# Kernel tuning notes

Hardware: AMD Instinct MI355X
Metric: run time of the kernel (lower is better)

Reference implementation:

```python
import jax, jax.numpy as jnp
import numpy as np

D_MODEL = 1024
N_HEADS = 16
D_HEAD = D_MODEL // N_HEADS
D_FF = 4096
EPS = 1e-5


def _layernorm(x, g, b):
    mu = jnp.mean(x, axis=-1, keepdims=True)
    var = jnp.mean(jnp.square(x - mu), axis=-1, keepdims=True)
    return (x - mu) * jax.lax.rsqrt(var + EPS) * g + b


def setup_inputs() -> dict:
    key = jax.random.key(0)
    ks = jax.random.split(key, 16)
    B, S, D = 2, 2048, D_MODEL

    def xavier(k, shape):
        fan_in, fan_out = shape[0], shape[1]
        lim = float(np.sqrt(6.0 / (fan_in + fan_out)))
        return jax.random.uniform(k, shape, jnp.float32, -lim, lim)

    return {
        "x": jax.random.normal(ks[0], (B, S, D), jnp.float32),
        "ln1_g": jnp.ones((D,), jnp.float32),
        "ln1_b": jnp.zeros((D,), jnp.float32),
        "wq": xavier(ks[1], (D, D)), "bq": jnp.zeros((D,), jnp.float32),
        "wk": xavier(ks[2], (D, D)), "bk": jnp.zeros((D,), jnp.float32),
        "wv": xavier(ks[3], (D, D)), "bv": jnp.zeros((D,), jnp.float32),
        "wo": xavier(ks[4], (D, D)), "bo": jnp.zeros((D,), jnp.float32),
        "wf": xavier(ks[5], (D, N_HEADS)), "bf": jnp.zeros((N_HEADS,), jnp.float32),
        "ln2_g": jnp.ones((D,), jnp.float32),
        "ln2_b": jnp.zeros((D,), jnp.float32),
        "w1": xavier(ks[6], (D, D_FF)), "b1": jnp.zeros((D_FF,), jnp.float32),
        "w2": xavier(ks[7], (D_FF, D)), "b2": jnp.zeros((D,), jnp.float32),
    }


def reference(x, ln1_g, ln1_b, wq, bq, wk, bk, wv, bv, wo, bo, wf, bf,
              ln2_g, ln2_b, w1, b1, w2, b2):
    B, S, D = x.shape
    H, Dh = N_HEADS, D_HEAD

    # --- pre-norm forgetting attention ---
    h = _layernorm(x, ln1_g, ln1_b)
    q = (h @ wq + bq).reshape(B, S, H, Dh)
    k = (h @ wk + bk).reshape(B, S, H, Dh)
    v = (h @ wv + bv).reshape(B, S, H, Dh)

    # per-head scalar forget gate f_t in (0,1); cumulative log-decay c_t
    logf = jax.nn.log_sigmoid(h @ wf + bf)           # (B, S, H)
    c = jnp.cumsum(logf, axis=1)                     # (B, S, H)

    scale = 1.0 / jnp.sqrt(jnp.asarray(Dh, x.dtype))
    logits = jnp.einsum("bihd,bjhd->bhij", q, k) * scale
    # decay bias D_ij = c_i - c_j (sum of log forget gates in (j, i])
    decay = c.transpose(0, 2, 1)                     # (B, H, S)
    logits = logits + decay[:, :, :, None] - decay[:, :, None, :]

    causal = jnp.tril(jnp.ones((S, S), bool))
    logits = jnp.where(causal[None, None], logits, -jnp.inf)

    attn = jax.nn.softmax(logits, axis=-1)           # (B, H, S, S)
    ctx = jnp.einsum("bhij,bjhd->bihd", attn, v).reshape(B, S, D)
    attn_out = ctx @ wo + bo

    x = x + attn_out                                 # dropout = identity (eval)

    # --- pre-norm GELU MLP ---
    h2 = _layernorm(x, ln2_g, ln2_b)
    ff = jax.nn.gelu(h2 @ w1 + b1, approximate=False) @ w2 + b2
    return x + ff
```

## Files before the change

### kernel.cpp

```cpp
#include <hip/hip_runtime.h>
#include <hip/hip_bf16.h>
#include <math.h>

typedef unsigned short u16;
typedef unsigned int u32;
typedef __bf16 bf16x8 __attribute__((ext_vector_type(8)));
typedef float f32x4 __attribute__((ext_vector_type(4)));
typedef u32 u32x4 __attribute__((ext_vector_type(4)));

__device__ __forceinline__ u16 f2bf(float f) {
  __hip_bfloat16 h = __float2bfloat16(f);
  return *reinterpret_cast<u16*>(&h);
}
__device__ __forceinline__ float bf2f(u16 u) {
  return __uint_as_float(((u32)u) << 16);
}

#define GLL(gp, lp)                                                     \
  __builtin_amdgcn_global_load_lds(                                     \
      (const __attribute__((address_space(1))) void*)(gp),              \
      (__attribute__((address_space(3))) void*)(lp), 16, 0, 0)

__global__ __launch_bounds__(256) void transpose_cast(
    const float* __restrict__ in, u16* __restrict__ out, int R, int C) {
  __shared__ float tile[32][33];
  int c0 = blockIdx.x * 32, r0 = blockIdx.y * 32;
  int tx = threadIdx.x & 31, ty = threadIdx.x >> 5;
  for (int i = ty; i < 32; i += 8) {
    int r = r0 + i, c = c0 + tx;
    if (r < R && c < C) tile[i][tx] = in[(size_t)r * C + c];
  }
  __syncthreads();
  for (int i = ty; i < 32; i += 8) {
    int c = c0 + i, r = r0 + tx;
    if (c < C && r < R) out[(size_t)c * R + r] = f2bf(tile[tx][i]);
  }
}

__global__ __launch_bounds__(256) void pack3(
    const float* __restrict__ a, const float* __restrict__ b,
    const float* __restrict__ c, float* __restrict__ o, u32* __restrict__ ctr) {
  int t = blockIdx.x * 256 + threadIdx.x;
  if (t == 0) *ctr = 0u;
  if (t < 1024) o[t] = a[t];
  else if (t < 2048) o[t] = b[t - 1024];
  else if (t < 3072) o[t] = c[t - 2048];
}

__global__ __launch_bounds__(256) void ln_kernel(
    const float* __restrict__ x, const float* __restrict__ g,
    const float* __restrict__ bb, u16* __restrict__ out) {
  __shared__ float red[8];
  const int row = blockIdx.x;
  const float* xr = x + (size_t)row * 1024;
  f32x4 v = *(const f32x4*)(xr + threadIdx.x * 4);
  float s = v[0] + v[1] + v[2] + v[3];
  #pragma unroll
  for (int off = 32; off > 0; off >>= 1) s += __shfl_xor(s, off, 64);
  if ((threadIdx.x & 63) == 0) red[threadIdx.x >> 6] = s;
  __syncthreads();
  float mu = (red[0] + red[1] + red[2] + red[3]) * (1.0f / 1024.0f);
  f32x4 d;
  d[0] = v[0] - mu; d[1] = v[1] - mu; d[2] = v[2] - mu; d[3] = v[3] - mu;
  float sq = d[0]*d[0] + d[1]*d[1] + d[2]*d[2] + d[3]*d[3];
  #pragma unroll
  for (int off = 32; off > 0; off >>= 1) sq += __shfl_xor(sq, off, 64);
  if ((threadIdx.x & 63) == 0) red[4 + (threadIdx.x >> 6)] = sq;
  __syncthreads();
  float var = (red[4] + red[5] + red[6] + red[7]) * (1.0f / 1024.0f);
  float rstd = rsqrtf(var + 1e-5f);
  int cb = threadIdx.x * 4;
  #pragma unroll
  for (int e = 0; e < 4; ++e)
    out[(size_t)row * 1024 + cb + e] = f2bf(d[e] * rstd * g[cb + e] + bb[cb + e]);
}

__global__ __launch_bounds__(256) void gemm_bt(
    const u16* __restrict__ A, const u16* __restrict__ Bt,
    const float* __restrict__ bias, const float* __restrict__ res,
    void* __restrict__ outp, int M, int N, int K, int mode) {
  __shared__ u16 As[128 * 32];
  __shared__ u16 Bs[128 * 32];
  const int tid = threadIdx.x;
  const int m0 = blockIdx.y * 128, n0 = blockIdx.x * 128;
  const int wave = tid >> 6, lane = tid & 63;
  const int wm = (wave >> 1) * 64, wn = (wave & 1) * 64;
  const int lr = lane & 15, quad = lane >> 4;
  const int g0 = wave * 2;
  const int srow0 = g0 * 16 + (lane >> 2);
  const int scol = (lane & 3) * 8;
  const u16* Ag0 = A + (size_t)(m0 + srow0) * K + scol;
  const u16* Ag1 = A + (size_t)(m0 + srow0 + 16) * K + scol;
  const u16* Bg0 = Bt + (size_t)(n0 + srow0) * K + scol;
  const u16* Bg1 = Bt + (size_t)(n0 + srow0 + 16) * K + scol;
  u16* Al0 = As + g0 * 512;
  u16* Al1 = As + (g0 + 1) * 512;
  u16* Bl0 = Bs + g0 * 512;
  u16* Bl1 = Bs + (g0 + 1) * 512;

  f32x4 acc[4][4] = {};

  for (int k0 = 0; k0 < K; k0 += 32) {
    GLL(Ag0 + k0, Al0);
    GLL(Ag1 + k0, Al1);
    GLL(Bg0 + k0, Bl0);
    GLL(Bg1 + k0, Bl1);
    __syncthreads();
    bf16x8 af[4], bfr[4];
    #pragma unroll
    for (int t = 0; t < 4; ++t) {
      af[t]  = *(const bf16x8*)&As[(wm + t * 16 + lr) * 32 + quad * 8];
      bfr[t] = *(const bf16x8*)&Bs[(wn + t * 16 + lr) * 32 + quad * 8];
    }
    #pragma unroll
    for (int mt = 0; mt < 4; ++mt)
      #pragma unroll
      for (int nt = 0; nt < 4; ++nt)
        acc[mt][nt] = __builtin_amdgcn_mfma_f32_16x16x32_bf16(
            af[mt], bfr[nt], acc[mt][nt], 0, 0, 0);
    __syncthreads();
  }

  #pragma unroll
  for (int mt = 0; mt < 4; ++mt) {
    #pragma unroll
    for (int nt = 0; nt < 4; ++nt) {
      const int col = n0 + wn + nt * 16 + lr;
      const float bvv = bias[col];
      #pragma unroll
      for (int rr = 0; rr < 4; ++rr) {
        const int row = m0 + wm + mt * 16 + quad * 4 + rr;
        const size_t idx = (size_t)row * N + col;
        float v = acc[mt][nt][rr] + bvv;
        if (mode == 0) {
          ((float*)outp)[idx] = v;
        } else if (mode == 1) {
          ((float*)outp)[idx] = v + res[idx];
        } else if (mode == 2) {
          float gl = 0.5f * v * (1.0f + erff(v * 0.70710678118654752f));
          ((u16*)outp)[idx] = f2bf(gl);
        } else {
          ((u16*)outp)[idx] = f2bf(v);
        }
      }
    }
  }
}

__global__ __launch_bounds__(256) void gemm_n64(
    const u16* __restrict__ A, const u16* __restrict__ Bt,
    const float* __restrict__ bias, const float* __restrict__ res,
    void* __restrict__ outp, int M, int N, int K, int mode) {
  __shared__ u16 As[128 * 32];
  __shared__ u16 Bs[64 * 32];
  const int tid = threadIdx.x;
  const int m0 = blockIdx.y * 128, n0 = blockIdx.x * 64;
  const int wave = tid >> 6, lane = tid & 63;
  const int wm = (wave >> 1) * 64, wn = (wave & 1) * 32;
  const int lr = lane & 15, quad = lane >> 4;
  const int g0 = wave * 2;
  const int srow = lane >> 2;
  const int scol = (lane & 3) * 8;
  const u16* Ag0 = A + (size_t)(m0 + g0 * 16 + srow) * K + scol;
  const u16* Ag1 = A + (size_t)(m0 + g0 * 16 + 16 + srow) * K + scol;
  const u16* Bg  = Bt + (size_t)(n0 + wave * 16 + srow) * K + scol;
  u16* Al0 = As + g0 * 512;
  u16* Al1 = As + (g0 + 1) * 512;
  u16* Bl  = Bs + wave * 512;

  f32x4 acc[4][2] = {};

  for (int k0 = 0; k0 < K; k0 += 32) {
    GLL(Ag0 + k0, Al0);
    GLL(Ag1 + k0, Al1);
    GLL(Bg + k0, Bl);
    __syncthreads();
    bf16x8 af[4], bfr[2];
    #pragma unroll
    for (int t = 0; t < 4; ++t)
      af[t] = *(const bf16x8*)&As[(wm + t * 16 + lr) * 32 + quad * 8];
    #pragma unroll
    for (int t = 0; t < 2; ++t)
      bfr[t] = *(const bf16x8*)&Bs[(wn + t * 16 + lr) * 32 + quad * 8];
    #pragma unroll
    for (int mt = 0; mt < 4; ++mt)
      #pragma unroll
      for (int nt = 0; nt < 2; ++nt)
        acc[mt][nt] = __builtin_amdgcn_mfma_f32_16x16x32_bf16(
            af[mt], bfr[nt], acc[mt][nt], 0, 0, 0);
    __syncthreads();
  }

  #pragma unroll
  for (int mt = 0; mt < 4; ++mt) {
    #pragma unroll
    for (int nt = 0; nt < 2; ++nt) {
      const int col = n0 + wn + nt * 16 + lr;
      const float bvv = bias[col];
      #pragma unroll
      for (int rr = 0; rr < 4; ++rr) {
        const int row = m0 + wm + mt * 16 + quad * 4 + rr;
        const size_t idx = (size_t)row * N + col;
        float v = acc[mt][nt][rr] + bvv;
        if (mode == 0) {
          ((float*)outp)[idx] = v;
        } else if (mode == 1) {
          ((float*)outp)[idx] = v + res[idx];
        } else if (mode == 2) {
          float gl = 0.5f * v * (1.0f + erff(v * 0.70710678118654752f));
          ((u16*)outp)[idx] = f2bf(gl);
        } else {
          ((u16*)outp)[idx] = f2bf(v);
        }
      }
    }
  }
}

__global__ __launch_bounds__(64) void logf_kernel(
    const u16* __restrict__ h, const u16* __restrict__ wfT,
    const float* __restrict__ bfv, float* __restrict__ c) {
  const int row = blockIdx.x;
  const int lane = threadIdx.x;
  float acc[16];
  #pragma unroll
  for (int n = 0; n < 16; ++n) acc[n] = 0.f;
  for (int t = 0; t < 16; ++t) {
    int kidx = t * 64 + lane;
    float hv = bf2f(h[(size_t)row * 1024 + kidx]);
    #pragma unroll
    for (int n = 0; n < 16; ++n)
      acc[n] += hv * bf2f(wfT[n * 1024 + kidx]);
  }
  float z = 0.f;
  #pragma unroll
  for (int n = 0; n < 16; ++n) {
    float r = acc[n];
    #pragma unroll
    for (int off = 1; off < 64; off <<= 1) r += __shfl_xor(r, off, 64);
    if (lane == n) z = r;
  }
  if (lane < 16) {
    z += bfv[lane];
    float lf = (z >= 0.f) ? -log1pf(expf(-z)) : (z - log1pf(expf(z)));
    c[(size_t)row * 16 + lane] = lf;
  }
}

__global__ __launch_bounds__(64) void cumsum_kernel(float* __restrict__ c, int S) {
  const int b = blockIdx.x >> 4, h = blockIdx.x & 15;
  const int lane = threadIdx.x;
  float carry = 0.f;
  for (int s0 = 0; s0 < S; s0 += 64) {
    float v = c[(size_t)(b * S + s0 + lane) * 16 + h];
    #pragma unroll
    for (int off = 1; off < 64; off <<= 1) {
      float t = __shfl_up(v, off, 64);
      if (lane >= off) v += t;
    }
    v += carry;
    c[(size_t)(b * S + s0 + lane) * 16 + h] = v;
    carry = __shfl(v, 63, 64);
  }
}

__global__ __launch_bounds__(256) void vtrans(
    const u16* __restrict__ qkvb, u16* __restrict__ vtg) {
  __shared__ u16 t[32][33];
  const int bh = blockIdx.z, b = bh >> 4, h = bh & 15;
  const int s0 = blockIdx.x * 32, d0 = blockIdx.y * 32;
  const int tx = threadIdx.x & 31, ty = threadIdx.x >> 5;
  for (int i = ty; i < 32; i += 8)
    t[i][tx] = qkvb[(size_t)(b * 2048 + s0 + i) * 3072 + 2048 + h * 64 + d0 + tx];
  __syncthreads();
  for (int i = ty; i < 32; i += 8)
    vtg[(size_t)(bh * 64 + d0 + i) * 2048 + s0 + tx] = t[tx][i];
}

#define FS 72
#define NITEMS 1024

__global__ __launch_bounds__(256) void fattn(
    const u16* __restrict__ qkvb, const u16* __restrict__ vtg,
    const float* __restrict__ c, u16* __restrict__ ctx, u32* __restrict__ ctr) {
  __shared__ u16 Qs[64 * FS];
  __shared__ u16 Ks[64 * FS];
  __shared__ u16 Vt[64 * FS];
  __shared__ u16 Ps[64 * FS];
  __shared__ float cjs[64];
  __shared__ u32 sh_item;
  const int S = 2048;
  const int tid = threadIdx.x, wave = tid >> 6, lane = tid & 63;
  const int lr = lane & 15, quad = lane >> 4;
  const int w16 = wave * 16;

  for (;;) {
    if (tid == 0) sh_item = atomicAdd(ctr, 1u);
    __syncthreads();
    const u32 item = sh_item;
    if (item >= NITEMS) return;
    const int qt = 31 - (int)(item >> 5);
    const int bh = (int)(item & 31), b = bh >> 4, h = bh & 15;
    const int i0 = qt * 64;

    {
      const int r = tid >> 2, cc = (tid & 3) * 16;
      const u16* src = qkvb + (size_t)(b * S + i0 + r) * 3072 + h * 64 + cc;
      *(u32x4*)&Qs[r * FS + cc] = *(const u32x4*)src;
      *(u32x4*)&Qs[r * FS + cc + 8] = *(const u32x4*)(src + 8);
    }
    float ci[4], m_[4], l_[4], alpha[4];
    f32x4 o_[4];
    #pragma unroll
    for (int r = 0; r < 4; ++r) {
      ci[r] = c[(size_t)(b * S + i0 + w16 + quad * 4 + r) * 16 + h];
      m_[r] = -INFINITY;
      l_[r] = 0.f;
    }
    #pragma unroll
    for (int dt = 0; dt < 4; ++dt) o_[dt] = (f32x4){0.f, 0.f, 0.f, 0.f};

    const int ntiles = qt + 1;
    for (int jt = 0; jt < ntiles; ++jt) {
      const int j0 = jt * 64;
      __syncthreads();
      {
        const int r = tid >> 2, cc = (tid & 3) * 16;
        const u16* ks = qkvb + (size_t)(b * S + j0 + r) * 3072 + 1024 + h * 64 + cc;
        *(u32x4*)&Ks[r * FS + cc] = *(const u32x4*)ks;
        *(u32x4*)&Ks[r * FS + cc + 8] = *(const u32x4*)(ks + 8);
        const u16* vs = vtg + (size_t)(bh * 64 + r) * 2048 + j0 + cc;
        *(u32x4*)&Vt[r * FS + cc] = *(const u32x4*)vs;
        *(u32x4*)&Vt[r * FS + cc + 8] = *(const u32x4*)(vs + 8);
        if (tid < 64) cjs[tid] = c[(size_t)(b * S + j0 + tid) * 16 + h];
      }
      __syncthreads();

      bf16x8 aq0 = *(const bf16x8*)&Qs[(w16 + lr) * FS + quad * 8];
      bf16x8 aq1 = *(const bf16x8*)&Qs[(w16 + lr) * FS + 32 + quad * 8];
      f32x4 sc[4];
      #pragma unroll
      for (int nt = 0; nt < 4; ++nt) {
        bf16x8 bk0 = *(const bf16x8*)&Ks[(nt * 16 + lr) * FS + quad * 8];
        bf16x8 bk1 = *(const bf16x8*)&Ks[(nt * 16 + lr) * FS + 32 + quad * 8];
        f32x4 z = {0.f, 0.f, 0.f, 0.f};
        z = __builtin_amdgcn_mfma_f32_16x16x32_bf16(aq0, bk0, z, 0, 0, 0);
        z = __builtin_amdgcn_mfma_f32_16x16x32_bf16(aq1, bk1, z, 0, 0, 0);
        sc[nt] = z;
      }
      const bool diag = (jt == qt);
      #pragma unroll
      for (int r = 0; r < 4; ++r) {
        const int i = i0 + w16 + quad * 4 + r;
        float lg[4], mrow = -INFINITY;
        #pragma unroll
        for (int nt = 0; nt < 4; ++nt) {
          const int j = j0 + nt * 16 + lr;
          float v = sc[nt][r] * 0.125f + ci[r] - cjs[nt * 16 + lr];
          if (diag && (j > i)) v = -INFINITY;
          lg[nt] = v;
          mrow = fmaxf(mrow, v);
        }
        #pragma unroll
        for (int off = 1; off < 16; off <<= 1)
          mrow = fmaxf(mrow, __shfl_xor(mrow, off, 64));
        const float mn = fmaxf(m_[r], mrow);
        alpha[r] = __expf(m_[r] - mn);
        m_[r] = mn;
        float rs = 0.f;
        #pragma unroll
        for (int nt = 0; nt < 4; ++nt) {
          const float p = __expf(lg[nt] - mn);
          Ps[(w16 + quad * 4 + r) * FS + nt * 16 + lr] = f2bf(p);
          rs += p;
        }
        #pragma unroll
        for (int off = 1; off < 16; off <<= 1) rs += __shfl_xor(rs, off, 64);
        l_[r] = l_[r] * alpha[r] + rs;
      }
      asm volatile("s_waitcnt lgkmcnt(0)" ::: "memory");
      #pragma unroll
      for (int dt = 0; dt < 4; ++dt)
        #pragma unroll
        for (int r = 0; r < 4; ++r) o_[dt][r] *= alpha[r];
      bf16x8 ap0 = *(const bf16x8*)&Ps[(w16 + lr) * FS + quad * 8];
      bf16x8 ap1 = *(const bf16x8*)&Ps[(w16 + lr) * FS + 32 + quad * 8];
      #pragma unroll
      for (int dt = 0; dt < 4; ++dt) {
        bf16x8 bv0 = *(const bf16x8*)&Vt[(dt * 16 + lr) * FS + quad * 8];
        bf16x8 bv1 = *(const bf16x8*)&Vt[(dt * 16 + lr) * FS + 32 + quad * 8];
        o_[dt] = __builtin_amdgcn_mfma_f32_16x16x32_bf16(ap0, bv0, o_[dt], 0, 0, 0);
        o_[dt] = __builtin_amdgcn_mfma_f32_16x16x32_bf16(ap1, bv1, o_[dt], 0, 0, 0);
      }
    }
    #pragma unroll
    for (int r = 0; r < 4; ++r) {
      const float inv = 1.0f / l_[r];
      const size_t base = (size_t)(b * S + i0 + w16 + quad * 4 + r) * 1024 + h * 64;
      #pragma unroll
      for (int dt = 0; dt < 4; ++dt)
        ctx[base + dt * 16 + lr] = f2bf(o_[dt][r] * inv);
    }
  }
}

extern "C" void kernel_launch(void* const* d_in, const int* in_sizes, int n_in,
                              void* d_out, int out_size, void* d_ws, size_t ws_size,
                              hipStream_t stream) {
  const float* x    = (const float*)d_in[0];
  const float* ln1g = (const float*)d_in[1];
  const float* ln1b = (const float*)d_in[2];
  const float* wq   = (const float*)d_in[3];
  const float* bq   = (const float*)d_in[4];
  const float* wk   = (const float*)d_in[5];
  const float* bk   = (const float*)d_in[6];
  const float* wv   = (const float*)d_in[7];
  const float* bv   = (const float*)d_in[8];
  const float* wo   = (const float*)d_in[9];
  const float* bo   = (const float*)d_in[10];
  const float* wf   = (const float*)d_in[11];
  const float* bfv  = (const float*)d_in[12];
  const float* ln2g = (const float*)d_in[13];
  const float* ln2b = (const float*)d_in[14];
  const float* w1   = (const float*)d_in[15];
  const float* b1   = (const float*)d_in[16];
  const float* w2   = (const float*)d_in[17];
  const float* b2   = (const float*)d_in[18];
  float* out = (float*)d_out;

  char* ws = (char*)d_ws;
  const size_t MB = 1024 * 1024;
  u16*   wqkvT = (u16*)(ws + 0 * MB);
  u16*   woT   = (u16*)(ws + 6 * MB);
  u16*   w1T   = (u16*)(ws + 8 * MB);
  u16*   w2T   = (u16*)(ws + 16 * MB);
  u16*   wfT   = (u16*)(ws + 24 * MB);
  float* bqkv  = (float*)(ws + 24 * MB + 65536);
  u32*   fctr  = (u32*)(ws + 24 * MB + 131072);
  u16*   hbuf  = (u16*)(ws + 25 * MB);
  u16*   ctx   = (u16*)(ws + 33 * MB);
  u16*   qkvb  = (u16*)(ws + 41 * MB);
  u16*   vtg   = (u16*)(ws + 65 * MB);
  float* cb    = (float*)(ws + 73 * MB);
  u16*   act1  = (u16*)(ws + 74 * MB);

  dim3 blk(256);
  transpose_cast<<<dim3(32, 32), blk, 0, stream>>>(wq, wqkvT, 1024, 1024);
  transpose_cast<<<dim3(32, 32), blk, 0, stream>>>(wk, wqkvT + 1024 * 1024, 1024, 1024);
  transpose_cast<<<dim3(32, 32), blk, 0, stream>>>(wv, wqkvT + 2 * 1024 * 1024, 1024, 1024);
  transpose_cast<<<dim3(32, 32), blk, 0, stream>>>(wo, woT, 1024, 1024);
  transpose_cast<<<dim3(128, 32), blk, 0, stream>>>(w1, w1T, 1024, 4096);
  transpose_cast<<<dim3(32, 128), blk, 0, stream>>>(w2, w2T, 4096, 1024);
  transpose_cast<<<dim3(1, 32), blk, 0, stream>>>(wf, wfT, 1024, 16);
  pack3<<<12, blk, 0, stream>>>(bq, bk, bv, bqkv, fctr);
  ln_kernel<<<4096, blk, 0, stream>>>(x, ln1g, ln1b, hbuf);
  gemm_bt<<<dim3(24, 32), blk, 0, stream>>>(hbuf, wqkvT, bqkv, nullptr, qkvb,
                                            4096, 3072, 1024, 3);
  logf_kernel<<<4096, dim3(64), 0, stream>>>(hbuf, wfT, bfv, cb);
  cumsum_kernel<<<32, dim3(64), 0, stream>>>(cb, 2048);
  vtrans<<<dim3(64, 2, 32), blk, 0, stream>>>(qkvb, vtg);
  fattn<<<dim3(512), blk, 0, stream>>>(qkvb, vtg, cb, ctx, fctr);
  gemm_n64<<<dim3(16, 32), blk, 0, stream>>>(ctx, woT, bo, x, out,
                                             4096, 1024, 1024, 1);
  ln_kernel<<<4096, blk, 0, stream>>>(out, ln2g, ln2b, hbuf);
  gemm_bt<<<dim3(32, 32), blk, 0, stream>>>(hbuf, w1T, b1, nullptr, act1,
                                            4096, 4096, 1024, 2);
  gemm_n64<<<dim3(16, 32), blk, 0, stream>>>(act1, w2T, b2, out, out,
                                             4096, 1024, 4096, 1);
}
```

Baseline: 533.6 us.

## Prefetch next K/V tile into registers and defer row-sum reduction in flash attention

The attention kernel now loads the next K, V^T and decay tile into registers while the current tile is computed, then writes them to shared memory at the top of the next iteration, hiding global load latency. Q fragments are hoisted out of the tile loop. Softmax switches to exp2 with log2e folded into the scale and decay terms. The per-tile row-sum shuffle reduction is deferred to a single reduction at the end. This adds register pressure and an extra barrier per tile in exchange for fewer stalls and shuffles.

```diff
diff --git a/kernel.cpp b/kernel.cpp
--- a/kernel.cpp
+++ b/kernel.cpp
@@ -279,6 +279,7 @@
 
 #define FS 72
 #define NITEMS 1024
+#define L2E 1.4426950408889634f
 
 __global__ __launch_bounds__(256) void fattn(
     const u16* __restrict__ qkvb, const u16* __restrict__ vtg,
@@ -293,6 +294,7 @@
   const int tid = threadIdx.x, wave = tid >> 6, lane = tid & 63;
   const int lr = lane & 15, quad = lane >> 4;
   const int w16 = wave * 16;
+  const int sr = tid >> 2, scc = (tid & 3) * 16;
 
   for (;;) {
     if (tid == 0) sh_item = atomicAdd(ctr, 1u);
@@ -304,40 +306,56 @@
     const int i0 = qt * 64;
 
     {
-      const int r = tid >> 2, cc = (tid & 3) * 16;
-      const u16* src = qkvb + (size_t)(b * S + i0 + r) * 3072 + h * 64 + cc;
-      *(u32x4*)&Qs[r * FS + cc] = *(const u32x4*)src;
-      *(u32x4*)&Qs[r * FS + cc + 8] = *(const u32x4*)(src + 8);
+      const u16* src = qkvb + (size_t)(b * S + i0 + sr) * 3072 + h * 64 + scc;
+      *(u32x4*)&Qs[sr * FS + scc] = *(const u32x4*)src;
+      *(u32x4*)&Qs[sr * FS + scc + 8] = *(const u32x4*)(src + 8);
+    }
+    u32x4 kr0, kr1, vr0, vr1;
+    float cjr = 0.f;
+    {
+      const u16* ks = qkvb + (size_t)(b * S + sr) * 3072 + 1024 + h * 64 + scc;
+      kr0 = *(const u32x4*)ks;
+      kr1 = *(const u32x4*)(ks + 8);
+      const u16* vs = vtg + (size_t)(bh * 64 + sr) * 2048 + scc;
+      vr0 = *(const u32x4*)vs;
+      vr1 = *(const u32x4*)(vs + 8);
+      if (tid < 64) cjr = c[(size_t)(b * S + tid) * 16 + h];
     }
     float ci[4], m_[4], l_[4], alpha[4];
     f32x4 o_[4];
     #pragma unroll
     for (int r = 0; r < 4; ++r) {
-      ci[r] = c[(size_t)(b * S + i0 + w16 + quad * 4 + r) * 16 + h];
+      ci[r] = c[(size_t)(b * S + i0 + w16 + quad * 4 + r) * 16 + h] * L2E;
       m_[r] = -INFINITY;
       l_[r] = 0.f;
     }
     #pragma unroll
     for (int dt = 0; dt < 4; ++dt) o_[dt] = (f32x4){0.f, 0.f, 0.f, 0.f};
+
+    __syncthreads();
+    const bf16x8 aq0 = *(const bf16x8*)&Qs[(w16 + lr) * FS + quad * 8];
+    const bf16x8 aq1 = *(const bf16x8*)&Qs[(w16 + lr) * FS + 32 + quad * 8];
 
     const int ntiles = qt + 1;
     for (int jt = 0; jt < ntiles; ++jt) {
       const int j0 = jt * 64;
+      *(u32x4*)&Ks[sr * FS + scc] = kr0;
+      *(u32x4*)&Ks[sr * FS + scc + 8] = kr1;
+      *(u32x4*)&Vt[sr * FS + scc] = vr0;
+      *(u32x4*)&Vt[sr * FS + scc + 8] = vr1;
+      if (tid < 64) cjs[tid] = cjr * L2E;
+      if (jt + 1 < ntiles) {
+        const int j1 = j0 + 64;
+        const u16* ks = qkvb + (size_t)(b * S + j1 + sr) * 3072 + 1024 + h * 64 + scc;
+        kr0 = *(const u32x4*)ks;
+        kr1 = *(const u32x4*)(ks + 8);
+        const u16* vs = vtg + (size_t)(bh * 64 + sr) * 2048 + j1 + scc;
+        vr0 = *(const u32x4*)vs;
+        vr1 = *(const u32x4*)(vs + 8);
+        if (tid < 64) cjr = c[(size_t)(b * S + j1 + tid) * 16 + h];
+      }
       __syncthreads();
-      {
-        const int r = tid >> 2, cc = (tid & 3) * 16;
-        const u16* ks = qkvb + (size_t)(b * S + j0 + r) * 3072 + 1024 + h * 64 + cc;
-        *(u32x4*)&Ks[r * FS + cc] = *(const u32x4*)ks;
-        *(u32x4*)&Ks[r * FS + cc + 8] = *(const u32x4*)(ks + 8);
-        const u16* vs = vtg + (size_t)(bh * 64 + r) * 2048 + j0 + cc;
-        *(u32x4*)&Vt[r * FS + cc] = *(const u32x4*)vs;
-        *(u32x4*)&Vt[r * FS + cc + 8] = *(const u32x4*)(vs + 8);
-        if (tid < 64) cjs[tid] = c[(size_t)(b * S + j0 + tid) * 16 + h];
-      }
-      __syncthreads();
-
-      bf16x8 aq0 = *(const bf16x8*)&Qs[(w16 + lr) * FS + quad * 8];
-      bf16x8 aq1 = *(const bf16x8*)&Qs[(w16 + lr) * FS + 32 + quad * 8];
+
       f32x4 sc[4];
       #pragma unroll
       for (int nt = 0; nt < 4; ++nt) {
@@ -356,7 +374,7 @@
         #pragma unroll
         for (int nt = 0; nt < 4; ++nt) {
           const int j = j0 + nt * 16 + lr;
-          float v = sc[nt][r] * 0.125f + ci[r] - cjs[nt * 16 + lr];
+          float v = sc[nt][r] * (0.125f * L2E) + ci[r] - cjs[nt * 16 + lr];
           if (diag && (j > i)) v = -INFINITY;
           lg[nt] = v;
           mrow = fmaxf(mrow, v);
@@ -365,17 +383,15 @@
         for (int off = 1; off < 16; off <<= 1)
           mrow = fmaxf(mrow, __shfl_xor(mrow, off, 64));
         const float mn = fmaxf(m_[r], mrow);
-        alpha[r] = __expf(m_[r] - mn);
+        alpha[r] = __builtin_exp2f(m_[r] - mn);
         m_[r] = mn;
         float rs = 0.f;
         #pragma unroll
         for (int nt = 0; nt < 4; ++nt) {
-          const float p = __expf(lg[nt] - mn);
+          const float p = __builtin_exp2f(lg[nt] - mn);
           Ps[(w16 + quad * 4 + r) * FS + nt * 16 + lr] = f2bf(p);
           rs += p;
         }
-        #pragma unroll
-        for (int off = 1; off < 16; off <<= 1) rs += __shfl_xor(rs, off, 64);
         l_[r] = l_[r] * alpha[r] + rs;
       }
       asm volatile("s_waitcnt lgkmcnt(0)" ::: "memory");
@@ -392,10 +408,14 @@
         o_[dt] = __builtin_amdgcn_mfma_f32_16x16x32_bf16(ap0, bv0, o_[dt], 0, 0, 0);
         o_[dt] = __builtin_amdgcn_mfma_f32_16x16x32_bf16(ap1, bv1, o_[dt], 0, 0, 0);
       }
+      __syncthreads();
     }
     #pragma unroll
     for (int r = 0; r < 4; ++r) {
-      const float inv = 1.0f / l_[r];
+      float lt = l_[r];
+      #pragma unroll
+      for (int off = 1; off < 16; off <<= 1) lt += __shfl_xor(lt, off, 64);
+      const float inv = 1.0f / lt;
       const size_t base = (size_t)(b * S + i0 + w16 + quad * 4 + r) * 1024 + h * 64;
       #pragma unroll
       for (int dt = 0; dt < 4; ++dt)
```

New measurement: 528.7 us. About the same (-0.9%).
